# Optimization experiments

Hardware: AMD Instinct MI355X
Metric: run time of the kernel (lower is better)

## Reference

```python
import jax, jax.numpy as jnp
import numpy as np

D_MODEL = 64
N_HEAD = 4
HEAD_DIM = D_MODEL // N_HEAD  # 16


def setup_inputs() -> dict:
    key = jax.random.key(0)
    ks = jax.random.split(key, 8)
    B, T_dec, T_enc = 16, 1024, 1024
    s = 1.0 / np.sqrt(D_MODEL)
    return {
        "x": jax.random.normal(ks[0], (B, T_dec, D_MODEL), dtype=jnp.float32),
        "encoder_outputs": jax.random.normal(ks[1], (B, T_enc, D_MODEL), dtype=jnp.float32),
        "encoder_outputs_mask": jnp.ones((B, T_enc), dtype=jnp.int32),
        "Wkv": jax.random.normal(ks[2], (D_MODEL, 2 * D_MODEL), dtype=jnp.float32) * s,
        "bkv": jnp.zeros((2 * D_MODEL,), dtype=jnp.float32),
        "Wq": jax.random.normal(ks[3], (D_MODEL, D_MODEL), dtype=jnp.float32) * s,
        "bq": jnp.zeros((D_MODEL,), dtype=jnp.float32),
        "Wproj": jax.random.normal(ks[4], (D_MODEL, D_MODEL), dtype=jnp.float32) * s,
        "bproj": jnp.zeros((D_MODEL,), dtype=jnp.float32),
    }


def reference(x, encoder_outputs, encoder_outputs_mask, Wkv, bkv, Wq, bq, Wproj, bproj):
    B, T_dec, C = x.shape
    T_enc = encoder_outputs.shape[1]
    kv = encoder_outputs @ Wkv + bkv                      # [B, T_enc, 2C]
    k, v = kv[..., :D_MODEL], kv[..., D_MODEL:]          # [B, T_enc, C]
    q = x @ Wq + bq                                      # [B, T_dec, C]
    q = q.reshape(B, T_dec, N_HEAD, HEAD_DIM)
    k = k.reshape(B, T_enc, N_HEAD, HEAD_DIM)
    v = v.reshape(B, T_enc, N_HEAD, HEAD_DIM)
    scale = 1.0 / jnp.sqrt(jnp.asarray(HEAD_DIM, dtype=q.dtype))
    att = jnp.einsum("bqhd,bkhd->bhqk", q, k) * scale    # [B, H, T_dec, T_enc]
    mask = (encoder_outputs_mask == 0)[:, None, None, :]  # [B, 1, 1, T_enc]
    att = jnp.where(mask, jnp.asarray(-jnp.inf, dtype=att.dtype), att)
    att = jax.nn.softmax(att, axis=-1)
    ctx = jnp.einsum("bhqk,bkhd->bqhd", att, v).reshape(B, T_dec, C)
    # dropout is identity at eval time
    return ctx @ Wproj + bproj
```

## Files before the change

### kernel.cpp

```cpp
#include <hip/hip_runtime.h>
#include <hip/hip_bf16.h>
#include <math.h>

#define DM 64
#define NH 4
#define HD 16
#define BATCH 16
#define TSEQ 1024

typedef short bf16x8 __attribute__((ext_vector_type(8)));
typedef float f32x16 __attribute__((ext_vector_type(16)));

static __device__ inline short f2bf(float x) {
    __hip_bfloat16 h = __float2bfloat16(x);
    return __builtin_bit_cast(short, h);
}
static __device__ inline float bf2f(short s) {
    __hip_bfloat16 h = __builtin_bit_cast(__hip_bfloat16, s);
    return __bfloat162float(h);
}
static __device__ inline unsigned pack2bf(float a, float b) {
    const unsigned lo = (unsigned short)f2bf(a);
    const unsigned hi = (unsigned short)f2bf(b);
    return lo | (hi << 16);
}

__global__ __launch_bounds__(256) void proj_kernel(
    const float* __restrict__ x, const float* __restrict__ enc,
    const float* __restrict__ Wkv, const float* __restrict__ bkv,
    const float* __restrict__ Wq,  const float* __restrict__ bq,
    const int* __restrict__ mask,
    short* __restrict__ qhi, short* __restrict__ qlo,
    short* __restrict__ khi, short* __restrict__ klo,
    short* __restrict__ vtt)
{
    const int t = threadIdx.x;
    const int bid  = blockIdx.x;
    const int xcd  = bid & 7;
    const int slot = bid >> 3;
    const int rowblock = (slot & 3) * 8 + xcd;
    const int part     = slot >> 2;
    const int r0 = rowblock * 512 + t;

    const float* in; const float* W; const float* bias; int cb, ldw;
    if (part < 4)      { in = x;   W = Wq;  ldw = 64;  cb = part*16;          bias = bq;  }
    else if (part < 8) { in = enc; W = Wkv; ldw = 128; cb = (part-4)*16;      bias = bkv; }
    else               { in = enc; W = Wkv; ldw = 128; cb = 64 + (part-8)*16; bias = bkv; }

    const float4* row0 = (const float4*)(in + (size_t)r0 * 64);
    const float4* row1 = (const float4*)(in + (size_t)(r0 + 256) * 64);

    float4 xc[2][4];
    #pragma unroll
    for (int v4 = 0; v4 < 4; ++v4) { xc[0][v4] = row0[v4]; xc[1][v4] = row1[v4]; }

    __shared__ float wsl[64][16];
    #pragma unroll
    for (int idx = t; idx < 1024; idx += 256)
        wsl[idx >> 4][idx & 15] = W[(idx >> 4)*ldw + cb + (idx & 15)];
    __syncthreads();

    float acc[2][16];
    #pragma unroll
    for (int j = 0; j < 16; ++j) { float bj = bias[cb + j]; acc[0][j] = bj; acc[1][j] = bj; }

    for (int kc = 0; kc < 4; ++kc) {
        float4 xn[2][4];
        if (kc < 3) {
            #pragma unroll
            for (int v4 = 0; v4 < 4; ++v4) {
                xn[0][v4] = row0[(kc+1)*4 + v4];
                xn[1][v4] = row1[(kc+1)*4 + v4];
            }
        }
        #pragma unroll
        for (int i = 0; i < 16; ++i) {
            const int k = kc*16 + i;
            const float4 w0 = ((const float4*)&wsl[k][0])[0];
            const float4 w1 = ((const float4*)&wsl[k][0])[1];
            const float4 w2 = ((const float4*)&wsl[k][0])[2];
            const float4 w3 = ((const float4*)&wsl[k][0])[3];
            #pragma unroll
            for (int rr = 0; rr < 2; ++rr) {
                const float xv = ((const float*)&xc[rr][i >> 2])[i & 3];
                acc[rr][0]  += xv*w0.x; acc[rr][1]  += xv*w0.y; acc[rr][2]  += xv*w0.z; acc[rr][3]  += xv*w0.w;
                acc[rr][4]  += xv*w1.x; acc[rr][5]  += xv*w1.y; acc[rr][6]  += xv*w1.z; acc[rr][7]  += xv*w1.w;
                acc[rr][8]  += xv*w2.x; acc[rr][9]  += xv*w2.y; acc[rr][10] += xv*w2.z; acc[rr][11] += xv*w2.w;
                acc[rr][12] += xv*w3.x; acc[rr][13] += xv*w3.y; acc[rr][14] += xv*w3.z; acc[rr][15] += xv*w3.w;
            }
        }
        if (kc < 3) {
            #pragma unroll
            for (int v4 = 0; v4 < 4; ++v4) { xc[0][v4] = xn[0][v4]; xc[1][v4] = xn[1][v4]; }
        }
    }

    #pragma unroll
    for (int rr = 0; rr < 2; ++rr) {
        const int r = r0 + rr*256;
        const int b = r >> 10, trow = r & 1023;
        if (part < 8) {
            const float scale = (part < 4) ? 0.36067376022224085f : 1.0f;
            short* dh = (part < 4) ? qhi : khi;
            short* dl = (part < 4) ? qlo : klo;
            const int h = (part < 4) ? part : (part - 4);
            bf16x8 h0, h1, l0, l1;
            #pragma unroll
            for (int j = 0; j < 16; ++j) {
                float vf = acc[rr][j] * scale;
                short hb = f2bf(vf);
                short lb = f2bf(vf - bf2f(hb));
                if (j < 8) { h0[j] = hb; l0[j] = lb; }
                else       { h1[j-8] = hb; l1[j-8] = lb; }
            }
            size_t off = (((size_t)(b*NH + h))*TSEQ + trow)*HD;
            *(bf16x8*)(dh + off)     = h0;
            *(bf16x8*)(dh + off + 8) = h1;
            *(bf16x8*)(dl + off)     = l0;
            *(bf16x8*)(dl + off + 8) = l1;
        } else {
            const int h = part - 8;
            const float mb = (mask[b*TSEQ + trow] != 0) ? 1.0f : 0.0f;
            short* tile = vtt + ((size_t)(b*NH + h))*32768 + (size_t)(trow >> 5)*1024;
            const int kw = trow & 31;
            #pragma unroll
            for (int j = 0; j < 16; ++j)
                tile[j*32 + kw] = f2bf(acc[rr][j] * mb);
            tile[16*32 + kw] = (mb != 0.0f) ? (short)0x3F80 : (short)0;
        }
    }
}

__global__ __launch_bounds__(512) void attn_kernel(
    const short* __restrict__ qhi, const short* __restrict__ qlo,
    const short* __restrict__ khi, const short* __restrict__ klo,
    const short* __restrict__ vtt,
    const float* __restrict__ Wproj, const float* __restrict__ bproj,
    float* __restrict__ out)
{
    const int tid  = threadIdx.x;
    const int lane = tid & 63;
    const int wid  = __builtin_amdgcn_readfirstlane(tid >> 6);
    const int h  = wid & 3;
    const int ks = wid >> 2;
    const int bid  = blockIdx.x;
    const int xcd  = bid & 7;
    const int slot = bid >> 3;
    const int b    = (slot & 1) * 8 + xcd;
    const int qbase = (slot >> 1) * 32;
    const int l31 = lane & 31;
    const bool hf = (lane >> 5) != 0;

    __shared__ float Cbuf[2][32][67];
    __shared__ float Lbuf[2][NH][32];

    const size_t qoff = (((size_t)(b*NH + h))*TSEQ + qbase + l31)*HD + (hf ? 8 : 0);
    const bf16x8 qBh = *(const bf16x8*)(qhi + qoff);
    const bf16x8 qBl = *(const bf16x8*)(qlo + qoff);

    const short* khb = khi + (((size_t)(b*NH + h))*TSEQ + ks*512)*HD;
    const short* klb = klo + (((size_t)(b*NH + h))*TSEQ + ks*512)*HD;
    const short* vtb = vtt + ((size_t)(b*NH + h))*32768 + (size_t)ks*16384;

    f32x16 Cacc;
    #pragma unroll
    for (int i = 0; i < 16; ++i) Cacc[i] = 0.f;

    for (int step = 0; step < 16; ++step) {
        const int ko = step * 32;
        const bf16x8 kAh = *(const bf16x8*)(khb + (size_t)(ko + l31)*HD + (hf ? 8 : 0));
        const bf16x8 kAl = *(const bf16x8*)(klb + (size_t)(ko + l31)*HD + (hf ? 8 : 0));
        const short* tile = vtb + (size_t)step * 1024;
        const bf16x8 vA0 = *(const bf16x8*)(tile + l31*32 + (hf ? 8 : 0));
        const bf16x8 vA1 = *(const bf16x8*)(tile + l31*32 + 16 + (hf ? 8 : 0));

        f32x16 S;
        #pragma unroll
        for (int i = 0; i < 16; ++i) S[i] = 0.f;
        S = __builtin_amdgcn_mfma_f32_32x32x16_bf16(kAh, qBh, S, 0, 0, 0);
        S = __builtin_amdgcn_mfma_f32_32x32x16_bf16(kAh, qBl, S, 0, 0, 0);
        S = __builtin_amdgcn_mfma_f32_32x32x16_bf16(kAl, qBh, S, 0, 0, 0);

        float p[16];
        #pragma unroll
        for (int i = 0; i < 16; ++i) p[i] = __builtin_amdgcn_exp2f(S[i]);

        unsigned pk[8];
        #pragma unroll
        for (int i = 0; i < 8; ++i) pk[i] = pack2bf(p[2*i], p[2*i+1]);

        const unsigned sA = hf ? pk[0] : pk[2];
        const unsigned sB = hf ? pk[1] : pk[3];
        const unsigned sC = hf ? pk[4] : pk[6];
        const unsigned sD = hf ? pk[5] : pk[7];
        const unsigned rA = (unsigned)__shfl_xor((int)sA, 32);
        const unsigned rB = (unsigned)__shfl_xor((int)sB, 32);
        const unsigned rC = (unsigned)__shfl_xor((int)sC, 32);
        const unsigned rD = (unsigned)__shfl_xor((int)sD, 32);

        int4 b1, b2;
        b1.x = hf ? (int)rA    : (int)pk[0];
        b1.y = hf ? (int)rB    : (int)pk[1];
        b1.z = hf ? (int)pk[2] : (int)rA;
        b1.w = hf ? (int)pk[3] : (int)rB;
        b2.x = hf ? (int)rC    : (int)pk[4];
        b2.y = hf ? (int)rD    : (int)pk[5];
        b2.z = hf ? (int)pk[6] : (int)rC;
        b2.w = hf ? (int)pk[7] : (int)rD;
        const bf16x8 pB0 = __builtin_bit_cast(bf16x8, b1);
        const bf16x8 pB1 = __builtin_bit_cast(bf16x8, b2);

        Cacc = __builtin_amdgcn_mfma_f32_32x32x16_bf16(vA0, pB0, Cacc, 0, 0, 0);
        Cacc = __builtin_amdgcn_mfma_f32_32x32x16_bf16(vA1, pB1, Cacc, 0, 0, 0);
    }

    #pragma unroll
    for (int r = 0; r < 8; ++r) {
        const int d = (r & 3) + 8*(r >> 2) + (hf ? 4 : 0);
        Cbuf[ks][l31][h*HD + d] = Cacc[r];
    }
    if (!hf) Lbuf[ks][h][l31] = Cacc[8];
    __syncthreads();

    const int q   = tid >> 4;
    const int cbo = (tid & 15) * 4;
    float linv[NH];
    #pragma unroll
    for (int hh = 0; hh < NH; ++hh)
        linv[hh] = 1.0f / (Lbuf[0][hh][q] + Lbuf[1][hh][q]);

    float o0 = bproj[cbo], o1 = bproj[cbo+1], o2 = bproj[cbo+2], o3 = bproj[cbo+3];
    #pragma unroll
    for (int i = 0; i < 64; ++i) {
        const float cv = (Cbuf[0][q][i] + Cbuf[1][q][i]) * linv[i >> 4];
        const float4 wr = *(const float4*)(Wproj + i*DM + cbo);
        o0 += cv*wr.x; o1 += cv*wr.y; o2 += cv*wr.z; o3 += cv*wr.w;
    }
    float4 st; st.x = o0; st.y = o1; st.z = o2; st.w = o3;
    *(float4*)(out + ((size_t)b*TSEQ + qbase + q)*DM + cbo) = st;
}

extern "C" void kernel_launch(void* const* d_in, const int* in_sizes, int n_in,
                              void* d_out, int out_size, void* d_ws, size_t ws_size,
                              hipStream_t stream) {
    const float* x     = (const float*)d_in[0];
    const float* enc   = (const float*)d_in[1];
    const int*   mask  = (const int*)  d_in[2];
    const float* Wkv   = (const float*)d_in[3];
    const float* bkv   = (const float*)d_in[4];
    const float* Wq    = (const float*)d_in[5];
    const float* bq    = (const float*)d_in[6];
    const float* Wproj = (const float*)d_in[7];
    const float* bproj = (const float*)d_in[8];
    float* out = (float*)d_out;

    const size_t SZ = (size_t)BATCH*NH*TSEQ*HD;
    short* qhi = (short*)d_ws;
    short* qlo = qhi + SZ;
    short* khi = qlo + SZ;
    short* klo = khi + SZ;
    short* vtt = klo + SZ;

    proj_kernel<<<dim3(384), dim3(256), 0, stream>>>(
        x, enc, Wkv, bkv, Wq, bq, mask, qhi, qlo, khi, klo, vtt);
    attn_kernel<<<dim3(512), dim3(512), 0, stream>>>(
        qhi, qlo, khi, klo, vtt, Wproj, bproj, out);
}
```

Baseline: 114.5 us.

## Use one row per thread in projection and hand-roll bf16 conversions

The projection kernel now gives each thread a single row instead of two, and drops the XCD-aware block swizzle in favour of a plain 2D grid of 64x12 blocks. All 64 input floats are loaded up front, overlapping with the weight staging into shared memory, instead of being prefetched in chunks. The bf16 conversion helpers are replaced with bit-twiddling round-to-nearest-even code and a cheaper pack. The goal is more blocks in flight and fewer instructions per conversion, at the cost of each weight tile in shared memory being reused by fewer rows and of losing the L2 locality the swizzle provided.

Result: no change. 114.0 us (-0.4%).

```diff
diff --git a/kernel.cpp b/kernel.cpp
--- a/kernel.cpp
+++ b/kernel.cpp
@@ -11,18 +11,20 @@
 typedef short bf16x8 __attribute__((ext_vector_type(8)));
 typedef float f32x16 __attribute__((ext_vector_type(16)));
 
+static __device__ inline unsigned bfround(float x) {
+    unsigned u = __builtin_bit_cast(unsigned, x);
+    return u + 0x7fffu + ((u >> 16) & 1u);
+}
 static __device__ inline short f2bf(float x) {
-    __hip_bfloat16 h = __float2bfloat16(x);
-    return __builtin_bit_cast(short, h);
+    return (short)(bfround(x) >> 16);
 }
 static __device__ inline float bf2f(short s) {
-    __hip_bfloat16 h = __builtin_bit_cast(__hip_bfloat16, s);
-    return __bfloat162float(h);
+    unsigned u = ((unsigned)(unsigned short)s) << 16;
+    float f = __builtin_bit_cast(float, u);
+    return f;
 }
 static __device__ inline unsigned pack2bf(float a, float b) {
-    const unsigned lo = (unsigned short)f2bf(a);
-    const unsigned hi = (unsigned short)f2bf(b);
-    return lo | (hi << 16);
+    return (bfround(a) >> 16) | (bfround(b) & 0xffff0000u);
 }
 
 __global__ __launch_bounds__(256) void proj_kernel(
@@ -35,99 +37,69 @@
     short* __restrict__ vtt)
 {
     const int t = threadIdx.x;
-    const int bid  = blockIdx.x;
-    const int xcd  = bid & 7;
-    const int slot = bid >> 3;
-    const int rowblock = (slot & 3) * 8 + xcd;
-    const int part     = slot >> 2;
-    const int r0 = rowblock * 512 + t;
+    const int part = blockIdx.y;
+    const int r = blockIdx.x * 256 + t;
+    const int b = r >> 10, trow = r & 1023;
 
     const float* in; const float* W; const float* bias; int cb, ldw;
     if (part < 4)      { in = x;   W = Wq;  ldw = 64;  cb = part*16;          bias = bq;  }
     else if (part < 8) { in = enc; W = Wkv; ldw = 128; cb = (part-4)*16;      bias = bkv; }
     else               { in = enc; W = Wkv; ldw = 128; cb = 64 + (part-8)*16; bias = bkv; }
 
-    const float4* row0 = (const float4*)(in + (size_t)r0 * 64);
-    const float4* row1 = (const float4*)(in + (size_t)(r0 + 256) * 64);
-
-    float4 xc[2][4];
-    #pragma unroll
-    for (int v4 = 0; v4 < 4; ++v4) { xc[0][v4] = row0[v4]; xc[1][v4] = row1[v4]; }
-
     __shared__ float wsl[64][16];
-    #pragma unroll
     for (int idx = t; idx < 1024; idx += 256)
         wsl[idx >> 4][idx & 15] = W[(idx >> 4)*ldw + cb + (idx & 15)];
+
+    float4 xr[16];
+    const float4* inrow = (const float4*)(in + (size_t)r * 64);
+    #pragma unroll
+    for (int i = 0; i < 16; ++i) xr[i] = inrow[i];
     __syncthreads();
 
-    float acc[2][16];
-    #pragma unroll
-    for (int j = 0; j < 16; ++j) { float bj = bias[cb + j]; acc[0][j] = bj; acc[1][j] = bj; }
-
-    for (int kc = 0; kc < 4; ++kc) {
-        float4 xn[2][4];
-        if (kc < 3) {
-            #pragma unroll
-            for (int v4 = 0; v4 < 4; ++v4) {
-                xn[0][v4] = row0[(kc+1)*4 + v4];
-                xn[1][v4] = row1[(kc+1)*4 + v4];
-            }
+    float acc[16];
+    #pragma unroll
+    for (int j = 0; j < 16; ++j) acc[j] = bias[cb + j];
+    #pragma unroll
+    for (int k = 0; k < 64; ++k) {
+        const float xv = ((const float*)xr)[k];
+        const float4 w0 = ((const float4*)&wsl[k][0])[0];
+        const float4 w1 = ((const float4*)&wsl[k][0])[1];
+        const float4 w2 = ((const float4*)&wsl[k][0])[2];
+        const float4 w3 = ((const float4*)&wsl[k][0])[3];
+        acc[0]  += xv*w0.x; acc[1]  += xv*w0.y; acc[2]  += xv*w0.z; acc[3]  += xv*w0.w;
+        acc[4]  += xv*w1.x; acc[5]  += xv*w1.y; acc[6]  += xv*w1.z; acc[7]  += xv*w1.w;
+        acc[8]  += xv*w2.x; acc[9]  += xv*w2.y; acc[10] += xv*w2.z; acc[11] += xv*w2.w;
+        acc[12] += xv*w3.x; acc[13] += xv*w3.y; acc[14] += xv*w3.z; acc[15] += xv*w3.w;
+    }
+
+    if (part < 8) {
+        const float scale = (part < 4) ? 0.36067376022224085f : 1.0f;
+        short* dh = (part < 4) ? qhi : khi;
+        short* dl = (part < 4) ? qlo : klo;
+        const int h = (part < 4) ? part : (part - 4);
+        bf16x8 h0, h1, l0, l1;
+        #pragma unroll
+        for (int j = 0; j < 16; ++j) {
+            float vf = acc[j] * scale;
+            short hb = f2bf(vf);
+            short lb = f2bf(vf - bf2f(hb));
+            if (j < 8) { h0[j] = hb; l0[j] = lb; }
+            else       { h1[j-8] = hb; l1[j-8] = lb; }
         }
-        #pragma unroll
-        for (int i = 0; i < 16; ++i) {
-            const int k = kc*16 + i;
-            const float4 w0 = ((const float4*)&wsl[k][0])[0];
-            const float4 w1 = ((const float4*)&wsl[k][0])[1];
-            const float4 w2 = ((const float4*)&wsl[k][0])[2];
-            const float4 w3 = ((const float4*)&wsl[k][0])[3];
-            #pragma unroll
-            for (int rr = 0; rr < 2; ++rr) {
-                const float xv = ((const float*)&xc[rr][i >> 2])[i & 3];
-                acc[rr][0]  += xv*w0.x; acc[rr][1]  += xv*w0.y; acc[rr][2]  += xv*w0.z; acc[rr][3]  += xv*w0.w;
-                acc[rr][4]  += xv*w1.x; acc[rr][5]  += xv*w1.y; acc[rr][6]  += xv*w1.z; acc[rr][7]  += xv*w1.w;
-                acc[rr][8]  += xv*w2.x; acc[rr][9]  += xv*w2.y; acc[rr][10] += xv*w2.z; acc[rr][11] += xv*w2.w;
-                acc[rr][12] += xv*w3.x; acc[rr][13] += xv*w3.y; acc[rr][14] += xv*w3.z; acc[rr][15] += xv*w3.w;
-            }
-        }
-        if (kc < 3) {
-            #pragma unroll
-            for (int v4 = 0; v4 < 4; ++v4) { xc[0][v4] = xn[0][v4]; xc[1][v4] = xn[1][v4]; }
-        }
-    }
-
-    #pragma unroll
-    for (int rr = 0; rr < 2; ++rr) {
-        const int r = r0 + rr*256;
-        const int b = r >> 10, trow = r & 1023;
-        if (part < 8) {
-            const float scale = (part < 4) ? 0.36067376022224085f : 1.0f;
-            short* dh = (part < 4) ? qhi : khi;
-            short* dl = (part < 4) ? qlo : klo;
-            const int h = (part < 4) ? part : (part - 4);
-            bf16x8 h0, h1, l0, l1;
-            #pragma unroll
-            for (int j = 0; j < 16; ++j) {
-                float vf = acc[rr][j] * scale;
-                short hb = f2bf(vf);
-                short lb = f2bf(vf - bf2f(hb));
-                if (j < 8) { h0[j] = hb; l0[j] = lb; }
-                else       { h1[j-8] = hb; l1[j-8] = lb; }
-            }
-            size_t off = (((size_t)(b*NH + h))*TSEQ + trow)*HD;
-            *(bf16x8*)(dh + off)     = h0;
-            *(bf16x8*)(dh + off + 8) = h1;
-            *(bf16x8*)(dl + off)     = l0;
-            *(bf16x8*)(dl + off + 8) = l1;
-        } else {
-            const int h = part - 8;
-            const float mb = (mask[b*TSEQ + trow] != 0) ? 1.0f : 0.0f;
-            short* tile = vtt + ((size_t)(b*NH + h))*32768 + (size_t)(trow >> 5)*1024;
-            const int kw = trow & 31;
-            #pragma unroll
-            for (int j = 0; j < 16; ++j)
-                tile[j*32 + kw] = f2bf(acc[rr][j] * mb);
-            tile[16*32 + kw] = (mb != 0.0f) ? (short)0x3F80 : (short)0;
-        }
+        size_t off = (((size_t)(b*NH + h))*TSEQ + trow)*HD;
+        *(bf16x8*)(dh + off)     = h0;
+        *(bf16x8*)(dh + off + 8) = h1;
+        *(bf16x8*)(dl + off)     = l0;
+        *(bf16x8*)(dl + off + 8) = l1;
+    } else {
+        const int h = part - 8;
+        const float mb = (mask[b*TSEQ + trow] != 0) ? 1.0f : 0.0f;
+        short* tile = vtt + ((size_t)(b*NH + h))*32768 + (size_t)(trow >> 5)*1024;
+        const int kw = trow & 31;
+        #pragma unroll
+        for (int j = 0; j < 16; ++j)
+            tile[j*32 + kw] = f2bf(acc[j] * mb);
+        tile[16*32 + kw] = (mb != 0.0f) ? (short)0x3F80 : (short)0;
     }
 }
 
@@ -261,7 +233,7 @@
     short* klo = khi + SZ;
     short* vtt = klo + SZ;
 
-    proj_kernel<<<dim3(384), dim3(256), 0, stream>>>(
+    proj_kernel<<<dim3(64, 12), dim3(256), 0, stream>>>(
         x, enc, Wkv, bkv, Wq, bq, mask, qhi, qlo, khi, klo, vtt);
     attn_kernel<<<dim3(512), dim3(512), 0, stream>>>(
         qhi, qlo, khi, klo, vtt, Wproj, bproj, out);
```
